# Kernel tuning notes

Measured on AMD Instinct MI355X. Metric: run time of the kernel, lower is better.

Reference implementation:

```python
import jax, jax.numpy as jnp
import numpy as np

B, S, DIN, DOUT = 4, 2048, 4096, 4096

def setup_inputs() -> dict:
    key = jax.random.key(0)
    k1, k2, k3, k4 = jax.random.split(key, 4)
    x = jax.random.normal(k1, (B, S, DIN), dtype=jnp.float32)
    # symmetric int8 weight values in [-127, 127]
    quantized_weight = jax.random.randint(k2, (DOUT, DIN), -127, 128, dtype=jnp.int32).astype(jnp.int8)
    weight_scale = jax.random.uniform(k3, (), dtype=jnp.float32) * 0.01 + 1e-4
    bias = jax.random.normal(k4, (DOUT,), dtype=jnp.float32)
    return {"x": x, "quantized_weight": quantized_weight, "weight_scale": weight_scale, "bias": bias}

def reference(x, quantized_weight, weight_scale, bias) -> jnp.ndarray:
    # dequantize_tensor: (q.float() - 0) * scale
    weight_fp32 = quantized_weight.astype(jnp.float32) * weight_scale  # [DOUT, DIN]
    # nn.functional.linear: x @ W^T + b
    return jnp.einsum('bsi,oi->bso', x, weight_fp32) + bias
```

## Files before the change

kernel.cpp:

```cpp
#include <hip/hip_runtime.h>
#include <stdint.h>
#include <stddef.h>

constexpr int MDIM = 8192;
constexpr int NDIM = 4096;
constexpr int KDIM = 4096;

using f32x4 = __attribute__((ext_vector_type(4))) float;
using s16x4 = __attribute__((ext_vector_type(4))) short;
using i32x4 = __attribute__((ext_vector_type(4))) int;

__device__ __forceinline__ short f32_to_bf16_rn(float f) {
  union { float f; uint32_t u; } v; v.f = f;
  uint32_t r = (v.u + 0x7FFFu + ((v.u >> 16) & 1u)) >> 16;
  return (short)(uint16_t)r;
}

__global__ void __launch_bounds__(256) quant_x_kernel(const float* __restrict__ in,
                                                      signed char* __restrict__ out,
                                                      float* __restrict__ sx) {
  const int row = blockIdx.x;
  const int t   = threadIdx.x;
  const float* rp = in + (size_t)row * KDIM;
  f32x4 v[4];
  float m = 0.0f;
#pragma unroll
  for (int j = 0; j < 4; ++j) {
    v[j] = *(const f32x4*)(rp + t * 16 + j * 4);
#pragma unroll
    for (int e = 0; e < 4; ++e) m = fmaxf(m, __builtin_fabsf(v[j][e]));
  }
#pragma unroll
  for (int off = 32; off > 0; off >>= 1) m = fmaxf(m, __shfl_xor(m, off, 64));
  __shared__ float wmax[4];
  const int wv = t >> 6, ln = t & 63;
  if (ln == 0) wmax[wv] = m;
  __syncthreads();
  m = fmaxf(fmaxf(wmax[0], wmax[1]), fmaxf(wmax[2], wmax[3]));
  const float inv = (m > 0.0f) ? (127.0f / m) : 0.0f;
  if (t == 0) sx[row] = m * (1.0f / 127.0f);
  i32x4 o;
#pragma unroll
  for (int j = 0; j < 4; ++j) {
    int b[4];
#pragma unroll
    for (int e = 0; e < 4; ++e) {
      int q = (int)rintf(v[j][e] * inv);
      q = q < -127 ? -127 : (q > 127 ? 127 : q);
      b[e] = q & 255;
    }
    o[j] = b[0] | (b[1] << 8) | (b[2] << 16) | (b[3] << 24);
  }
  *(i32x4*)(out + (size_t)row * KDIM + t * 16) = o;
}

__global__ void __launch_bounds__(256) quant_w_kernel(const int* __restrict__ in,
                                                      signed char* __restrict__ out, int n16) {
  int i = blockIdx.x * 256 + threadIdx.x;
  const int stride = gridDim.x * 256;
  for (; i < n16; i += stride) {
    const i32x4* p = (const i32x4*)(in + (size_t)i * 16);
    i32x4 o;
#pragma unroll
    for (int j = 0; j < 4; ++j) {
      i32x4 a = p[j];
      o[j] = (a[0] & 255) | ((a[1] & 255) << 8) | ((a[2] & 255) << 16) | ((a[3] & 255) << 24);
    }
    *(i32x4*)(out + (size_t)i * 16) = o;
  }
}


#define BAR asm volatile("s_barrier" ::: "memory")
#define WAITVM(n) asm volatile("s_waitcnt vmcnt(" #n ")" ::: "memory")
#define SGB(mask, n) __builtin_amdgcn_sched_group_barrier((mask), (n), 0)

#define GLL(src, dst) __builtin_amdgcn_global_load_lds(                     \
    (const __attribute__((address_space(1))) void*)(src),                   \
    (__attribute__((address_space(3))) void*)(dst), 16, 0, 0)

#define STGP(tau) do {                                                      \
  GLL(Arow + (size_t)r0 * 4096 + (tau) * 64 + cb,                           \
      lds + (tau) * 32768 + t * 16);                                        \
  GLL(Arow + (size_t)(128 + r0) * 4096 + (tau) * 64 + cb,                   \
      lds + (tau) * 32768 + 8192 + t * 16);                                 \
  GLL(Brow + (size_t)r0 * 4096 + (tau) * 64 + cb,                           \
      lds + (tau) * 32768 + 16384 + t * 16);                                \
  GLL(Brow + (size_t)(128 + r0) * 4096 + (tau) * 64 + cb,                   \
      lds + (tau) * 32768 + 16384 + 8192 + t * 16);                         \
} while (0)

#define STGL(u3) do {                                                       \
  GLL(aSrc0, lds + (u3) * 32768 + t * 16);                                  \
  GLL(aSrc1, lds + (u3) * 32768 + 8192 + t * 16);                           \
  GLL(bSrc0, lds + (u3) * 32768 + 16384 + t * 16);                          \
  GLL(bSrc1, lds + (u3) * 32768 + 16384 + 8192 + t * 16);                   \
  aSrc0 += 64; aSrc1 += 64; bSrc0 += 64; bSrc1 += 64;                       \
} while (0)

#define LDA8(u, fi) (*(const i32x4*)(lds + (u) * 32768                      \
    + (wm * 8 + (fi)) * 1024 + laneoff))
#define LDB8(u, j)  (*(const i32x4*)(lds + (u) * 32768 + 16384              \
    + (wn * 4 + (j)) * 1024 + laneoff))

#define WIN(u, AFC, BFC, AFN, BFN, dord, dostg, vmarg) do {                 \
  __builtin_amdgcn_s_setprio(1);                                            \
  if (dord) {                                                               \
    _Pragma("unroll") for (int i_ = 0; i_ < 8; ++i_)                        \
      AFN[i_] = LDA8(((u) + 1) & 3, i_);                                    \
    _Pragma("unroll") for (int j_ = 0; j_ < 4; ++j_)                        \
      BFN[j_] = LDB8(((u) + 1) & 3, j_);                                    \
  }                                                                         \
  if (dostg) STGL(((u) + 3) & 3);                                           \
  _Pragma("unroll") for (int i_ = 0; i_ < 8; ++i_)                          \
  _Pragma("unroll") for (int j_ = 0; j_ < 4; ++j_)                          \
    acc[i_][j_] = __builtin_amdgcn_mfma_i32_16x16x64_i8(                    \
        AFC[i_], BFC[j_], acc[i_][j_], 0, 0, 0);                            \
  __builtin_amdgcn_s_setprio(0);                                            \
  if ((dord) && (dostg)) {                                                  \
    SGB(0x100, 3); SGB(0x20, 1); SGB(0x8, 8);                               \
    SGB(0x100, 3); SGB(0x20, 1); SGB(0x8, 8);                               \
    SGB(0x100, 3); SGB(0x20, 1); SGB(0x8, 8);                               \
    SGB(0x100, 3); SGB(0x20, 1); SGB(0x8, 8);                               \
  }                                                                         \
  if ((vmarg) == 4) { WAITVM(4); } else if ((vmarg) == 0) { WAITVM(0); }    \
  BAR;                                                                      \
} while (0)

__global__ void __launch_bounds__(512, 1) gemm_i8_ring_ilv(
    const signed char* __restrict__ A, const signed char* __restrict__ Bw,
    const float* __restrict__ sx, const float* __restrict__ scale_p,
    const float* __restrict__ bias, float* __restrict__ out) {
  __shared__ __align__(16) char lds[131072];

  const int t      = threadIdx.x;
  const int lane   = t & 63;
  const int wave   = t >> 6;
  const int wm     = wave >> 2;
  const int wn     = wave & 3;
  const int lane15 = lane & 15;
  const int lh     = lane >> 4;

  const int laneoff = (lane15 * 64 + lh * 16) ^ ((lane15 & 8) << 2);

  const int ax = ((t >> 5) & 1) << 5;
  const int a0 = (t * 16) ^ ax;
  const int r0 = a0 >> 6;
  const int cb = a0 & 63;

  const int bid   = blockIdx.x;
  const int wg    = (bid & 7) * 64 + (bid >> 3);
  const int ntile = wg & 15;
  const int mtile = wg >> 4;
  const int m0 = mtile * 256;
  const int n0 = ntile * 256;

  const char* Arow = (const char*)(A + (size_t)m0 * KDIM);
  const char* Brow = (const char*)(Bw + (size_t)n0 * KDIM);

  const char* aSrc0 = Arow + (size_t)r0 * 4096 + 192 + cb;
  const char* aSrc1 = Arow + (size_t)(128 + r0) * 4096 + 192 + cb;
  const char* bSrc0 = Brow + (size_t)r0 * 4096 + 192 + cb;
  const char* bSrc1 = Brow + (size_t)(128 + r0) * 4096 + 192 + cb;

  i32x4 acc[8][4] = {};
  i32x4 afE[8], afO[8], bfE[4], bfO[4];

  STGP(0);
  STGP(1);
  STGP(2);
  WAITVM(8);
  BAR;
#pragma unroll
  for (int i_ = 0; i_ < 8; ++i_) afE[i_] = LDA8(0, i_);
#pragma unroll
  for (int j_ = 0; j_ < 4; ++j_) bfE[j_] = LDB8(0, j_);
  WAITVM(4);
  BAR;

#pragma unroll 1
  for (int tp = 0; tp < 15; ++tp) {
    WIN(0, afE, bfE, afO, bfO, 1, 1, 4);
    WIN(1, afO, bfO, afE, bfE, 1, 1, 4);
    WIN(2, afE, bfE, afO, bfO, 1, 1, 4);
    WIN(3, afO, bfO, afE, bfE, 1, 1, 4);
  }
  WIN(0, afE, bfE, afO, bfO, 1, 1, 4);
  WIN(1, afO, bfO, afE, bfE, 1, 0, 0);
  WIN(2, afE, bfE, afO, bfO, 1, 0, -1);
  WIN(3, afO, bfO, afE, bfE, 0, 0, -1);

  const float sw = scale_p[0];
  float bv[4];
#pragma unroll
  for (int j = 0; j < 4; ++j) bv[j] = bias[n0 + wn * 64 + j * 16 + lane15];
#pragma unroll
  for (int i = 0; i < 8; ++i) {
    const int rowb = m0 + wm * 128 + i * 16 + lh * 4;
    float sxq[4];
#pragma unroll
    for (int q = 0; q < 4; ++q) sxq[q] = sx[rowb + q] * sw;
#pragma unroll
    for (int j = 0; j < 4; ++j) {
      const int col = n0 + wn * 64 + j * 16 + lane15;
#pragma unroll
      for (int q = 0; q < 4; ++q)
        out[(size_t)(rowb + q) * NDIM + col] = (float)acc[i][j][q] * sxq[q] + bv[j];
    }
  }
}

constexpr int FTILE = 128;
constexpr int FBK   = 64;

__global__ void __launch_bounds__(256) gemm_raw(
    const float* __restrict__ X, const int* __restrict__ W,
    const float* __restrict__ scale_p, const float* __restrict__ bias,
    float* __restrict__ out) {
  __shared__ short As[FTILE * FBK];
  __shared__ short Bs[FTILE * FBK];

  const int t      = threadIdx.x;
  const int lane   = t & 63;
  const int wave   = t >> 6;
  const int wm     = wave >> 1;
  const int wn     = wave & 1;
  const int lane15   = lane & 15;
  const int laneHalf = lane >> 4;

  const int bid   = blockIdx.x;
  const int wg    = (bid & 7) * 256 + (bid >> 3);
  const int ntile = wg & 31;
  const int mtile = wg >> 5;
  const int m0 = mtile * FTILE;
  const int n0 = ntile * FTILE;

  f32x4 acc[4][4] = {};

  for (int k0 = 0; k0 < KDIM; k0 += FBK) {
    __syncthreads();
#pragma unroll
    for (int r = 0; r < 8; ++r) {
      const int f   = r * 256 + t;
      const int row = f >> 4;
      const int c4  = (f & 15) * 4;
      f32x4 v = *(const f32x4*)(X + (size_t)(m0 + row) * KDIM + (k0 + c4));
      s16x4 h;
#pragma unroll
      for (int j = 0; j < 4; ++j) h[j] = f32_to_bf16_rn(v[j]);
      *(s16x4*)&As[row * FBK + c4] = h;

      i32x4 wv = *(const i32x4*)(W + (size_t)(n0 + row) * KDIM + (k0 + c4));
      s16x4 hw;
#pragma unroll
      for (int j = 0; j < 4; ++j) hw[j] = f32_to_bf16_rn((float)wv[j]);
      *(s16x4*)&Bs[row * FBK + c4] = hw;
    }
    __syncthreads();

#pragma unroll
    for (int kk = 0; kk < FBK; kk += 32) {
      const int kb = kk + laneHalf * 8;
      using s16x8f = __attribute__((ext_vector_type(8))) short;
      s16x8f af[4], bf[4];
#pragma unroll
      for (int i = 0; i < 4; ++i) {
        af[i] = *(const s16x8f*)&As[(wm * 64 + i * 16 + lane15) * FBK + kb];
        bf[i] = *(const s16x8f*)&Bs[(wn * 64 + i * 16 + lane15) * FBK + kb];
      }
#pragma unroll
      for (int i = 0; i < 4; ++i)
#pragma unroll
        for (int j = 0; j < 4; ++j)
          acc[i][j] = __builtin_amdgcn_mfma_f32_16x16x32_bf16(af[i], bf[j], acc[i][j], 0, 0, 0);
    }
  }

  const float s = scale_p[0];
#pragma unroll
  for (int j = 0; j < 4; ++j) {
    const int col = n0 + wn * 64 + j * 16 + lane15;
    const float bv = bias[col];
#pragma unroll
    for (int i = 0; i < 4; ++i) {
      const int row = m0 + wm * 64 + i * 16 + laneHalf * 4;
#pragma unroll
      for (int q = 0; q < 4; ++q)
        out[(size_t)(row + q) * NDIM + col] = acc[i][j][q] * s + bv;
    }
  }
}

extern "C" void kernel_launch(void* const* d_in, const int* in_sizes, int n_in,
                              void* d_out, int out_size, void* d_ws, size_t ws_size,
                              hipStream_t stream) {
  const float* x     = (const float*)d_in[0];
  const int*   w     = (const int*)d_in[1];
  const float* scale = (const float*)d_in[2];
  const float* bias  = (const float*)d_in[3];
  float* out = (float*)d_out;

  const size_t a_bytes = (size_t)MDIM * KDIM;
  const size_t b_bytes = (size_t)NDIM * KDIM;
  const size_t need    = a_bytes + b_bytes + MDIM * 4;

  if (ws_size >= need) {
    signed char* Ai8 = (signed char*)d_ws;
    signed char* Bi8 = Ai8 + a_bytes;
    float*       sxp = (float*)(Bi8 + b_bytes);
    quant_x_kernel<<<MDIM, 256, 0, stream>>>(x, Ai8, sxp);
    quant_w_kernel<<<4096, 256, 0, stream>>>(w, Bi8, (int)(b_bytes / 16));
    const int nwg = (MDIM / 256) * (NDIM / 256);
    gemm_i8_ring_ilv<<<nwg, 512, 0, stream>>>(Ai8, Bi8, sxp, scale, bias, out);
  } else {
    const int nwg = (MDIM / FTILE) * (NDIM / FTILE);
    gemm_raw<<<nwg, 256, 0, stream>>>(x, w, scale, bias, out);
  }
}
```

Before: 182.3 us.

## Use four waves with 128x128 per-wave tiles in int8 GEMM

Halves the workgroup from 512 to 256 threads and gives each wave a 128x128 output sub-tile (8x8 MFMA fragments) instead of 128x64. Each thread now issues eight global-to-LDS loads per stage, and the wait counts and sched-group barriers are retuned to match. Each wave gets more MFMA work per LDS fragment read, which is meant to raise arithmetic intensity and cut LDS traffic. In exchange there are fewer waves to hide latency, and the accumulator plus fragment registers roughly double, which risks spills.

Result: slower. 186.8 us (+2.5%).

```diff
diff --git a/kernel.cpp b/kernel.cpp
--- a/kernel.cpp
+++ b/kernel.cpp
@@ -82,52 +82,69 @@
 #define STGP(tau) do {                                                      \
   GLL(Arow + (size_t)r0 * 4096 + (tau) * 64 + cb,                           \
       lds + (tau) * 32768 + t * 16);                                        \
-  GLL(Arow + (size_t)(128 + r0) * 4096 + (tau) * 64 + cb,                   \
+  GLL(Arow + (size_t)(r0 + 64) * 4096 + (tau) * 64 + cb,                    \
+      lds + (tau) * 32768 + 4096 + t * 16);                                 \
+  GLL(Arow + (size_t)(r0 + 128) * 4096 + (tau) * 64 + cb,                   \
       lds + (tau) * 32768 + 8192 + t * 16);                                 \
+  GLL(Arow + (size_t)(r0 + 192) * 4096 + (tau) * 64 + cb,                   \
+      lds + (tau) * 32768 + 12288 + t * 16);                                \
   GLL(Brow + (size_t)r0 * 4096 + (tau) * 64 + cb,                           \
       lds + (tau) * 32768 + 16384 + t * 16);                                \
-  GLL(Brow + (size_t)(128 + r0) * 4096 + (tau) * 64 + cb,                   \
+  GLL(Brow + (size_t)(r0 + 64) * 4096 + (tau) * 64 + cb,                    \
+      lds + (tau) * 32768 + 16384 + 4096 + t * 16);                         \
+  GLL(Brow + (size_t)(r0 + 128) * 4096 + (tau) * 64 + cb,                   \
       lds + (tau) * 32768 + 16384 + 8192 + t * 16);                         \
+  GLL(Brow + (size_t)(r0 + 192) * 4096 + (tau) * 64 + cb,                   \
+      lds + (tau) * 32768 + 16384 + 12288 + t * 16);                        \
 } while (0)
 
 #define STGL(u3) do {                                                       \
-  GLL(aSrc0, lds + (u3) * 32768 + t * 16);                                  \
-  GLL(aSrc1, lds + (u3) * 32768 + 8192 + t * 16);                           \
-  GLL(bSrc0, lds + (u3) * 32768 + 16384 + t * 16);                          \
-  GLL(bSrc1, lds + (u3) * 32768 + 16384 + 8192 + t * 16);                   \
-  aSrc0 += 64; aSrc1 += 64; bSrc0 += 64; bSrc1 += 64;                       \
+  GLL(aP0, lds + (u3) * 32768 + t * 16);                                    \
+  GLL(aP1, lds + (u3) * 32768 + 4096 + t * 16);                             \
+  GLL(aP2, lds + (u3) * 32768 + 8192 + t * 16);                             \
+  GLL(aP3, lds + (u3) * 32768 + 12288 + t * 16);                            \
+  GLL(bP0, lds + (u3) * 32768 + 16384 + t * 16);                            \
+  GLL(bP1, lds + (u3) * 32768 + 16384 + 4096 + t * 16);                     \
+  GLL(bP2, lds + (u3) * 32768 + 16384 + 8192 + t * 16);                     \
+  GLL(bP3, lds + (u3) * 32768 + 16384 + 12288 + t * 16);                    \
+  aP0 += 64; aP1 += 64; aP2 += 64; aP3 += 64;                               \
+  bP0 += 64; bP1 += 64; bP2 += 64; bP3 += 64;                               \
 } while (0)
 
 #define LDA8(u, fi) (*(const i32x4*)(lds + (u) * 32768                      \
     + (wm * 8 + (fi)) * 1024 + laneoff))
-#define LDB8(u, j)  (*(const i32x4*)(lds + (u) * 32768 + 16384              \
-    + (wn * 4 + (j)) * 1024 + laneoff))
+#define LDB8(u, fj) (*(const i32x4*)(lds + (u) * 32768 + 16384              \
+    + (wn * 8 + (fj)) * 1024 + laneoff))
 
 #define WIN(u, AFC, BFC, AFN, BFN, dord, dostg, vmarg) do {                 \
   __builtin_amdgcn_s_setprio(1);                                            \
   if (dord) {                                                               \
     _Pragma("unroll") for (int i_ = 0; i_ < 8; ++i_)                        \
       AFN[i_] = LDA8(((u) + 1) & 3, i_);                                    \
-    _Pragma("unroll") for (int j_ = 0; j_ < 4; ++j_)                        \
+    _Pragma("unroll") for (int j_ = 0; j_ < 8; ++j_)                        \
       BFN[j_] = LDB8(((u) + 1) & 3, j_);                                    \
   }                                                                         \
   if (dostg) STGL(((u) + 3) & 3);                                           \
   _Pragma("unroll") for (int i_ = 0; i_ < 8; ++i_)                          \
-  _Pragma("unroll") for (int j_ = 0; j_ < 4; ++j_)                          \
+  _Pragma("unroll") for (int j_ = 0; j_ < 8; ++j_)                          \
     acc[i_][j_] = __builtin_amdgcn_mfma_i32_16x16x64_i8(                    \
         AFC[i_], BFC[j_], acc[i_][j_], 0, 0, 0);                            \
   __builtin_amdgcn_s_setprio(0);                                            \
   if ((dord) && (dostg)) {                                                  \
-    SGB(0x100, 3); SGB(0x20, 1); SGB(0x8, 8);                               \
-    SGB(0x100, 3); SGB(0x20, 1); SGB(0x8, 8);                               \
-    SGB(0x100, 3); SGB(0x20, 1); SGB(0x8, 8);                               \
-    SGB(0x100, 3); SGB(0x20, 1); SGB(0x8, 8);                               \
+    SGB(0x100, 2); SGB(0x20, 1); SGB(0x8, 8);                               \
+    SGB(0x100, 2); SGB(0x20, 1); SGB(0x8, 8);                               \
+    SGB(0x100, 2); SGB(0x20, 1); SGB(0x8, 8);                               \
+    SGB(0x100, 2); SGB(0x20, 1); SGB(0x8, 8);                               \
+    SGB(0x100, 2); SGB(0x20, 1); SGB(0x8, 8);                               \
+    SGB(0x100, 2); SGB(0x20, 1); SGB(0x8, 8);                               \
+    SGB(0x100, 2); SGB(0x20, 1); SGB(0x8, 8);                               \
+    SGB(0x100, 2); SGB(0x20, 1); SGB(0x8, 8);                               \
   }                                                                         \
-  if ((vmarg) == 4) { WAITVM(4); } else if ((vmarg) == 0) { WAITVM(0); }    \
+  if ((vmarg) == 8) { WAITVM(8); } else if ((vmarg) == 0) { WAITVM(0); }    \
   BAR;                                                                      \
 } while (0)
 
-__global__ void __launch_bounds__(512, 1) gemm_i8_ring_ilv(
+__global__ void __launch_bounds__(256, 1) gemm_i8_mega(
     const signed char* __restrict__ A, const signed char* __restrict__ Bw,
     const float* __restrict__ sx, const float* __restrict__ scale_p,
     const float* __restrict__ bias, float* __restrict__ out) {
@@ -136,8 +153,8 @@
   const int t      = threadIdx.x;
   const int lane   = t & 63;
   const int wave   = t >> 6;
-  const int wm     = wave >> 2;
-  const int wn     = wave & 3;
+  const int wm     = wave >> 1;
+  const int wn     = wave & 1;
   const int lane15 = lane & 15;
   const int lh     = lane >> 4;
 
@@ -158,54 +175,58 @@
   const char* Arow = (const char*)(A + (size_t)m0 * KDIM);
   const char* Brow = (const char*)(Bw + (size_t)n0 * KDIM);
 
-  const char* aSrc0 = Arow + (size_t)r0 * 4096 + 192 + cb;
-  const char* aSrc1 = Arow + (size_t)(128 + r0) * 4096 + 192 + cb;
-  const char* bSrc0 = Brow + (size_t)r0 * 4096 + 192 + cb;
-  const char* bSrc1 = Brow + (size_t)(128 + r0) * 4096 + 192 + cb;
-
-  i32x4 acc[8][4] = {};
-  i32x4 afE[8], afO[8], bfE[4], bfO[4];
+  const char* aP0 = Arow + (size_t)r0 * 4096 + 192 + cb;
+  const char* aP1 = Arow + (size_t)(r0 + 64) * 4096 + 192 + cb;
+  const char* aP2 = Arow + (size_t)(r0 + 128) * 4096 + 192 + cb;
+  const char* aP3 = Arow + (size_t)(r0 + 192) * 4096 + 192 + cb;
+  const char* bP0 = Brow + (size_t)r0 * 4096 + 192 + cb;
+  const char* bP1 = Brow + (size_t)(r0 + 64) * 4096 + 192 + cb;
+  const char* bP2 = Brow + (size_t)(r0 + 128) * 4096 + 192 + cb;
+  const char* bP3 = Brow + (size_t)(r0 + 192) * 4096 + 192 + cb;
+
+  i32x4 acc[8][8] = {};
+  i32x4 afE[8], afO[8], bfE[8], bfO[8];
 
   STGP(0);
   STGP(1);
   STGP(2);
+  WAITVM(16);
+  BAR;
+#pragma unroll
+  for (int i_ = 0; i_ < 8; ++i_) afE[i_] = LDA8(0, i_);
+#pragma unroll
+  for (int j_ = 0; j_ < 8; ++j_) bfE[j_] = LDB8(0, j_);
   WAITVM(8);
   BAR;
-#pragma unroll
-  for (int i_ = 0; i_ < 8; ++i_) afE[i_] = LDA8(0, i_);
-#pragma unroll
-  for (int j_ = 0; j_ < 4; ++j_) bfE[j_] = LDB8(0, j_);
-  WAITVM(4);
-  BAR;
 
 #pragma unroll 1
   for (int tp = 0; tp < 15; ++tp) {
-    WIN(0, afE, bfE, afO, bfO, 1, 1, 4);
-    WIN(1, afO, bfO, afE, bfE, 1, 1, 4);
-    WIN(2, afE, bfE, afO, bfO, 1, 1, 4);
-    WIN(3, afO, bfO, afE, bfE, 1, 1, 4);
-  }
-  WIN(0, afE, bfE, afO, bfO, 1, 1, 4);
+    WIN(0, afE, bfE, afO, bfO, 1, 1, 8);
+    WIN(1, afO, bfO, afE, bfE, 1, 1, 8);
+    WIN(2, afE, bfE, afO, bfO, 1, 1, 8);
+    WIN(3, afO, bfO, afE, bfE, 1, 1, 8);
+  }
+  WIN(0, afE, bfE, afO, bfO, 1, 1, 8);
   WIN(1, afO, bfO, afE, bfE, 1, 0, 0);
   WIN(2, afE, bfE, afO, bfO, 1, 0, -1);
   WIN(3, afO, bfO, afE, bfE, 0, 0, -1);
 
   const float sw = scale_p[0];
-  float bv[4];
-#pragma unroll
-  for (int j = 0; j < 4; ++j) bv[j] = bias[n0 + wn * 64 + j * 16 + lane15];
-#pragma unroll
-  for (int i = 0; i < 8; ++i) {
-    const int rowb = m0 + wm * 128 + i * 16 + lh * 4;
+  float bv[8];
+#pragma unroll
+  for (int j = 0; j < 8; ++j) bv[j] = bias[n0 + wn * 128 + j * 16 + lane15];
+#pragma unroll
+  for (int fi = 0; fi < 8; ++fi) {
+    const int rowb = m0 + wm * 128 + fi * 16 + lh * 4;
     float sxq[4];
 #pragma unroll
     for (int q = 0; q < 4; ++q) sxq[q] = sx[rowb + q] * sw;
 #pragma unroll
-    for (int j = 0; j < 4; ++j) {
-      const int col = n0 + wn * 64 + j * 16 + lane15;
+    for (int fj = 0; fj < 8; ++fj) {
+      const int col = n0 + wn * 128 + fj * 16 + lane15;
 #pragma unroll
       for (int q = 0; q < 4; ++q)
-        out[(size_t)(rowb + q) * NDIM + col] = (float)acc[i][j][q] * sxq[q] + bv[j];
+        out[(size_t)(rowb + q) * NDIM + col] = (float)acc[fi][fj][q] * sxq[q] + bv[fj];
     }
   }
 }
@@ -311,7 +332,7 @@
     quant_x_kernel<<<MDIM, 256, 0, stream>>>(x, Ai8, sxp);
     quant_w_kernel<<<4096, 256, 0, stream>>>(w, Bi8, (int)(b_bytes / 16));
     const int nwg = (MDIM / 256) * (NDIM / 256);
-    gemm_i8_ring_ilv<<<nwg, 512, 0, stream>>>(Ai8, Bi8, sxp, scale, bias, out);
+    gemm_i8_mega<<<nwg, 256, 0, stream>>>(Ai8, Bi8, sxp, scale, bias, out);
   } else {
     const int nwg = (MDIM / FTILE) * (NDIM / FTILE);
     gemm_raw<<<nwg, 256, 0, stream>>>(x, w, scale, bias, out);
```
